# Performance work log

Hardware: AMD Instinct MI355X
Metric: run time of the kernel (lower is better)

Reference implementation:

```python
import jax, jax.numpy as jnp
import numpy as np

B, N, K, TC = 4, 4096, 16, 3
N_TAYLOR = 20  # 3rd-order Taylor monomials of (x,y,z): 1 + 3 + 6 + 10
CHANNELS = [(6, 32), (32, 64), (64, 128), (128, 256)]


def _taylor(rel):
    # rel: B,3,N,K relative coords -> B,20,N,K monomial basis up to degree 3
    x, y, z = rel[:, 0], rel[:, 1], rel[:, 2]
    one = jnp.ones_like(x)
    return jnp.stack([one, x, y, z,
                      x * x, x * y, x * z, y * y, y * z, z * z,
                      x * x * x, x * x * y, x * x * z, x * y * y, x * y * z,
                      x * z * z, y * y * y, y * y * z, y * z * z, z * z * z], axis=1)


def _group(feat, idx):
    # feat: B,C,N ; idx: B,N,K (int) -> B,C,N,K gathered neighbor features
    return jax.vmap(lambda f, i: f[:, i])(feat, idx)


def setup_inputs() -> dict:
    key = jax.random.key(0)
    ks = jax.random.split(key, 8)
    inp = {"pc": jax.random.normal(ks[0], (B, N, 6), dtype=jnp.float32)}
    for l, (cin, cout) in enumerate(CHANNELS, start=1):
        k1, k2 = jax.random.split(ks[l], 2)
        inp[f"w1_{l}"] = jax.random.normal(k1, (TC, N_TAYLOR), dtype=jnp.float32) * 0.1
        inp[f"b1_{l}"] = jnp.zeros((TC,), dtype=jnp.float32)
        fan_in = cin * TC * K
        inp[f"w2_{l}"] = jax.random.normal(k2, (cout, cin * TC, K), dtype=jnp.float32) * (1.0 / np.sqrt(fan_in))
        inp[f"b2_{l}"] = jnp.zeros((cout,), dtype=jnp.float32)
    return inp


def _forward(pc, params):
    pcT = pc.transpose(0, 2, 1)                 # B,6,N
    xyz = pcT[:, :3]                            # B,3,N
    # KNN graph: pairwise squared distances, top-k nearest (includes self)
    sq = jnp.sum(xyz * xyz, axis=1)             # B,N
    d2 = sq[:, :, None] + sq[:, None, :] - 2.0 * jnp.einsum('bcn,bcm->bnm', xyz, xyz)
    _, idx = jax.lax.top_k(-d2, K)              # B,N,K
    gxyz = _group(xyz, idx)                     # B,3,N,K
    rel = gxyz - xyz[:, :, :, None]             # B,3,N,K relative neighbor coords
    tay_basis = _taylor(rel)                    # B,20,N,K

    feat = pcT
    feats = []
    for (w1, b1, w2, b2) in params:
        # Taylor kernel weights: 1x1 conv over the 20 monomials -> TC channels
        tay = jnp.einsum('btnk,ct->bcnk', tay_basis, w1) + b1[None, :, None, None]  # B,TC,N,K
        gf = _group(feat, idx)                  # B,C,N,K
        C = gf.shape[1]
        fused = (gf[:, :, None] * tay[:, None]).reshape(B, C * TC, N, K)  # outer product
        # Conv2d(C*TC, out, kernel=(1,K)): contract channel and neighbor axes
        out = jnp.einsum('bcnk,ock->bon', fused, w2) + b2[None, :, None]
        feat = jax.nn.relu(out)                 # B,Cout,N
        feats.append(feat)

    point_feat = jnp.concatenate(feats, axis=1)  # B,480,N
    top2, _ = jax.lax.top_k(point_feat, 2)       # top-2 over N (last axis) -> B,480,2
    cat_feat = top2.reshape(B, -1)               # B,960
    return cat_feat, point_feat


def reference(pc, w1_1, b1_1, w2_1, b2_1, w1_2, b1_2, w2_2, b2_2,
              w1_3, b1_3, w2_3, b2_3, w1_4, b1_4, w2_4, b2_4):
    params = [(w1_1, b1_1, w2_1, b2_1), (w1_2, b1_2, w2_2, b2_2),
              (w1_3, b1_3, w2_3, b2_3), (w1_4, b1_4, w2_4, b2_4)]
    return _forward(pc, params)
```

## Files before the change

kernel.cpp:

```cpp
#include <hip/hip_runtime.h>
#include <hip/hip_fp16.h>
#include <cfloat>

#define BB 4
#define NN 4096
#define KK 16
#define NPTS (BB * NN)
#define NT48 (48 * NPTS)

typedef __attribute__((ext_vector_type(8))) _Float16 f16x8;
typedef __attribute__((ext_vector_type(4))) float f32x4;
typedef unsigned int u32;
typedef unsigned long long u64;

__device__ __forceinline__ short f2h(float v) {
  __half h = __float2half_rn(v);
  return __half_as_short(h);
}
__device__ __forceinline__ u32 mulh2(u32 a, __half2 t) {
  __half2 x = __hmul2(*(__half2*)&a, t);
  return *(u32*)&x;
}

__global__ __launch_bounds__(256) void pc2ft_kernel(const float* __restrict__ pc,
                                                    short* __restrict__ ft0,
                                                    float4* __restrict__ xyzq) {
  const int i = blockIdx.x * 256 + threadIdx.x;
  if (i >= NPTS) return;
  const float* s = pc + (size_t)i * 6;
  short* d = ft0 + (size_t)i * 8;
#pragma unroll
  for (int c = 0; c < 6; ++c) d[c] = f2h(s[c]);
  d[6] = 0; d[7] = 0;
  const float x = s[0], y = s[1], z = s[2];
  xyzq[i] = make_float4(x, y, z, fmaf(z, z, fmaf(y, y, x * x)));
}

__global__ __launch_bounds__(256) void knn_select(const float4* __restrict__ xyzq,
                                                  int* __restrict__ idx_out) {
  __shared__ float wT[4];
  __shared__ u64 list[128];
  __shared__ int lcnt;
  const int g = blockIdx.x;
  const int b = g >> 12;
  const int t = threadIdx.x;
  const int lane = t & 63;
  const float4* base = xyzq + (b << 12);
  const float4 q = xyzq[g];
  float d2v[16];
  float mymin = FLT_MAX;
#pragma unroll
  for (int i = 0; i < 16; ++i) {
    const float4 c = base[i * 256 + t];
    const float dot = fmaf(q.z, c.z, fmaf(q.y, c.y, q.x * c.x));
    d2v[i] = fmaf(-2.0f, dot, q.w + c.w);
    mymin = fminf(mymin, d2v[i]);
  }
  if (t == 0) lcnt = 0;
  float v = mymin;
#pragma unroll
  for (int k = 2; k <= 64; k <<= 1) {
#pragma unroll
    for (int j = k >> 1; j >= 1; j >>= 1) {
      const float o = __shfl_xor(v, j, 64);
      const bool take_min = (((lane & k) == 0) == ((lane & j) == 0));
      v = take_min ? fminf(v, o) : fmaxf(v, o);
    }
  }
  const float tw = __shfl(v, 15, 64);
  if (lane == 0) wT[t >> 6] = tw;
  __syncthreads();
  const float T = fminf(fminf(wT[0], wT[1]), fminf(wT[2], wT[3]));
#pragma unroll
  for (int i = 0; i < 16; ++i) {
    if (d2v[i] <= T) {
      const u32 bits = __float_as_uint(d2v[i]);
      const u32 key = bits ^ ((u32)((int)bits >> 31) | 0x80000000u);
      const int pos = atomicAdd(&lcnt, 1);
      if (pos < 128) list[pos] = ((u64)key << 32) | (u32)(i * 256 + t);
    }
  }
  __syncthreads();
  if (t < 128) {
    const int m = min(lcnt, 128);
    const u64 my = (t < m) ? list[t] : ~0ull;
    int rank = 0;
#pragma unroll 4
    for (int i = 0; i < m; ++i) rank += (list[i] < my) ? 1 : 0;
    if (t < m && rank < 16)
      idx_out[(size_t)g * KK + rank] = (int)(my & 0xFFFFFFFFull);
  }
}

__global__ __launch_bounds__(256) void wcvt_kernel(const float* __restrict__ w2,
                                                   short* __restrict__ wb,
                                                   int CIN, int COUT, int CPAD, int LOGC,
                                                   int total8) {
  const int i = blockIdx.x * 256 + threadIdx.x;
  if (i >= total8) return;
  const int q8 = i * 8;
  const int QT = CPAD * 48;
  const int o = q8 / QT;
  const int r = q8 - o * QT;
  const int kq = r >> LOGC;
  const int c0 = r & (CPAD - 1);
  const int tt = kq >> 4;
  const int k = kq & 15;
  short h[8];
#pragma unroll
  for (int j = 0; j < 8; ++j) {
    const int c = c0 + j;
    const float v = (o < COUT && c < CIN) ? w2[(size_t)o * CIN * 48 + (c * 3 + tt) * 16 + k] : 0.0f;
    h[j] = f2h(v);
  }
  short* d = wb + (size_t)o * QT + r;
#pragma unroll
  for (int j = 0; j < 8; ++j) d[j] = h[j];
}

__global__ __launch_bounds__(256) void taylor_kernel(
    const float* __restrict__ pc, const int* __restrict__ idx,
    const float* __restrict__ w1_1, const float* __restrict__ b1_1,
    const float* __restrict__ w1_2, const float* __restrict__ b1_2,
    const float* __restrict__ w1_3, const float* __restrict__ b1_3,
    const float* __restrict__ w1_4, const float* __restrict__ b1_4,
    float* __restrict__ tayg) {
  const int i = blockIdx.x * 256 + threadIdx.x;
  if (i >= NPTS * KK) return;
  const int p = i & (NPTS - 1);
  const int k = i >> 14;
  const int n = p & (NN - 1);
  const int b = p >> 12;
  const float* pcb = pc + (size_t)b * NN * 6;
  const int m = idx[(size_t)p * KK + k];
  const float x = pcb[m * 6 + 0] - pcb[n * 6 + 0];
  const float y = pcb[m * 6 + 1] - pcb[n * 6 + 1];
  const float z = pcb[m * 6 + 2] - pcb[n * 6 + 2];
  float tb[20];
  tb[0] = 1.0f; tb[1] = x; tb[2] = y; tb[3] = z;
  tb[4] = x * x; tb[5] = x * y; tb[6] = x * z;
  tb[7] = y * y; tb[8] = y * z; tb[9] = z * z;
  tb[10] = tb[4] * x; tb[11] = tb[4] * y; tb[12] = tb[4] * z;
  tb[13] = tb[5] * y; tb[14] = tb[5] * z; tb[15] = tb[6] * z;
  tb[16] = tb[7] * y; tb[17] = tb[7] * z; tb[18] = tb[8] * z; tb[19] = tb[9] * z;
  const float* w1s[4] = {w1_1, w1_2, w1_3, w1_4};
  const float* b1s[4] = {b1_1, b1_2, b1_3, b1_4};
#pragma unroll
  for (int l = 0; l < 4; ++l) {
    const float* w1 = w1s[l];
    const float* b1 = b1s[l];
#pragma unroll
    for (int c = 0; c < 3; ++c) {
      float s = b1[c];
#pragma unroll
      for (int j = 0; j < 20; ++j) s = fmaf(w1[c * 20 + j], tb[j], s);
      tayg[(size_t)(l * 48 + c * 16 + k) * NPTS + p] = s;
    }
  }
}

template <int CPAD, int LOGC, int COUT, int OTILE>
__global__ __launch_bounds__(256) void conv_mfma_kernel(
    const char* __restrict__ ftin,
    const short* __restrict__ wb,
    const float* __restrict__ b2,
    const float* __restrict__ tayg,
    const int* __restrict__ idx,
    float* __restrict__ pfout, int pfbstride,
    short* __restrict__ ftout, int CPADN) {
  constexpr int QTOT = CPAD * 48;
  constexpr int OUTER = QTOT / 64;
  constexpr int NJ = OTILE / 64;
  constexpr int PW = 16 * NJ;
  constexpr int NH = OTILE / 32;
  __shared__ __align__(16) short As[2][OTILE * 64];
  __shared__ __align__(16) short Bs[2][64 * 64];
  __shared__ __align__(16) unsigned short tayH[48 * 64];
  __shared__ int idxS[16 * 64];
  const int t = threadIdx.x;
  const int pbase = blockIdx.x * 64;
  const int obase = blockIdx.y * OTILE;
  const int b = pbase >> 12;
  const int nbase = pbase & (NN - 1);
  const int p_loc = t >> 2;
  const int sub = t & 3;
#pragma unroll
  for (int i = 0; i < 3; ++i) {
    const int f = i * 1024 + t * 4;
    const float4 tv4 = *(const float4*)&tayg[(size_t)(f >> 6) * NPTS + pbase + (f & 63)];
    ushort4 h4;
    h4.x = (unsigned short)f2h(tv4.x);
    h4.y = (unsigned short)f2h(tv4.y);
    h4.z = (unsigned short)f2h(tv4.z);
    h4.w = (unsigned short)f2h(tv4.w);
    *(ushort4*)&tayH[f] = h4;
  }
  {
    const int4 mi = *(const int4*)&idx[(size_t)(pbase + p_loc) * KK + sub * 4];
    const int gb = b << 12;
    idxS[(sub * 4 + 0) * 64 + p_loc] = (gb + mi.x) << (LOGC + 1);
    idxS[(sub * 4 + 1) * 64 + p_loc] = (gb + mi.y) << (LOGC + 1);
    idxS[(sub * 4 + 2) * 64 + p_loc] = (gb + mi.z) << (LOGC + 1);
    idxS[(sub * 4 + 3) * 64 + p_loc] = (gb + mi.w) << (LOGC + 1);
  }
  const int arow = t >> 3;
  const int apos = t & 7;
  const int aswz = (t >> 4) & 7;
  const short* awl[NH];
#pragma unroll
  for (int h = 0; h < NH; ++h)
    awl[h] = wb + (size_t)(obase + h * 32 + arow) * QTOT + ((apos ^ aswz) * 8);
  auto dmaA = [&](int o, int ph) {
#pragma unroll
    for (int h = 0; h < NH; ++h)
      __builtin_amdgcn_global_load_lds(
          (const __attribute__((address_space(1))) u32*)(awl[h] + o * 64),
          (__attribute__((address_space(3))) u32*)&As[ph][h * 2048 + t * 8], 16, 0, 0);
  };
  const int lane = t & 63;
  const int w = t >> 6;
  const int wm = (NJ == 2) ? (w & 1) : 0;
  const int wn = (NJ == 2) ? (w >> 1) : w;
  const int fr = lane & 15;
  const int fk = lane >> 4;
  const int rsw = (fr >> 1) & 7;
  const int bswz = (p_loc >> 1) & 7;
  f32x4 acc[4][NJ];
#pragma unroll
  for (int i = 0; i < 4; ++i)
#pragma unroll
    for (int j = 0; j < NJ; ++j) acc[i][j] = (f32x4)(0.0f);

  uint4 fv[2];
  unsigned short tvh[2];
  auto prefB = [&](int o) {
#pragma unroll
    for (int z = 0; z < 2; ++z) {
      const int q0 = o * 64 + z * 32 + sub * 8;
      const int kq = q0 >> LOGC;
      const int c0 = q0 & (CPAD - 1);
      const int moff = idxS[(kq & 15) * 64 + p_loc];
      tvh[z] = tayH[kq * 64 + p_loc];
      fv[z] = *(const uint4*)(ftin + moff + (c0 << 1));
    }
  };
  auto buildB = [&](int ph) {
#pragma unroll
    for (int z = 0; z < 2; ++z) {
      const __half2 t2 = __half2half2(__ushort_as_half(tvh[z]));
      const uint4 f = fv[z];
      uint4 r;
      r.x = mulh2(f.x, t2); r.y = mulh2(f.y, t2);
      r.z = mulh2(f.z, t2); r.w = mulh2(f.w, t2);
      const int pos = (z * 4 + sub) ^ bswz;
      *(uint4*)&Bs[ph][p_loc * 64 + pos * 8] = r;
    }
  };
  dmaA(0, 0);
  __syncthreads();
  prefB(0);
  buildB(0);
  __syncthreads();
#pragma unroll 1
  for (int o = 0; o < OUTER; ++o) {
    const int ph = o & 1;
    if (o + 1 < OUTER) { dmaA(o + 1, ph ^ 1); prefB(o + 1); }
#pragma unroll
    for (int z = 0; z < 2; ++z) {
      f16x8 af[4], bf[NJ];
      const int pos8 = ((z * 4 + fk) ^ rsw) * 8;
#pragma unroll
      for (int i = 0; i < 4; ++i)
        af[i] = *(const f16x8*)&As[ph][(wm * 64 + i * 16 + fr) * 64 + pos8];
#pragma unroll
      for (int j = 0; j < NJ; ++j)
        bf[j] = *(const f16x8*)&Bs[ph][(wn * PW + j * 16 + fr) * 64 + pos8];
#pragma unroll
      for (int i = 0; i < 4; ++i)
#pragma unroll
        for (int j = 0; j < NJ; ++j)
          acc[i][j] = __builtin_amdgcn_mfma_f32_16x16x32_f16(af[i], bf[j], acc[i][j], 0, 0, 0);
      if (z == 0 && o + 1 < OUTER) buildB(ph ^ 1);
    }
    if (o + 1 < OUTER) __syncthreads();
  }
  float* outb = pfout + (size_t)b * pfbstride;
#pragma unroll
  for (int i = 0; i < 4; ++i) {
    const int o0 = obase + wm * 64 + i * 16 + fk * 4;
    if (o0 < COUT) {
      const float4 b4 = *(const float4*)&b2[o0];
#pragma unroll
      for (int j = 0; j < NJ; ++j) {
        const int p_l = wn * PW + j * 16 + fr;
        const float v0 = fmaxf(acc[i][j][0] + b4.x, 0.0f);
        const float v1 = fmaxf(acc[i][j][1] + b4.y, 0.0f);
        const float v2 = fmaxf(acc[i][j][2] + b4.z, 0.0f);
        const float v3 = fmaxf(acc[i][j][3] + b4.w, 0.0f);
        outb[(size_t)(o0 + 0) * NN + nbase + p_l] = v0;
        outb[(size_t)(o0 + 1) * NN + nbase + p_l] = v1;
        outb[(size_t)(o0 + 2) * NN + nbase + p_l] = v2;
        outb[(size_t)(o0 + 3) * NN + nbase + p_l] = v3;
        if (ftout) {
          const __half2 h01 = __floats2half2_rn(v0, v1);
          const __half2 h23 = __floats2half2_rn(v2, v3);
          uint2 pk;
          pk.x = *(const u32*)&h01;
          pk.y = *(const u32*)&h23;
          *(uint2*)&ftout[(size_t)(pbase + p_l) * CPADN + o0] = pk;
        }
      }
    }
  }
}

__global__ __launch_bounds__(256) void top2_kernel(const float* __restrict__ pf,
                                                   float* __restrict__ cat) {
  const int row = blockIdx.x;
  const float* p = pf + (size_t)row * NN;
  float m1 = -FLT_MAX, m2 = -FLT_MAX;
  for (int i = threadIdx.x; i < NN; i += 256) {
    const float v = p[i];
    if (v > m1) { m2 = m1; m1 = v; }
    else if (v > m2) m2 = v;
  }
#pragma unroll
  for (int off = 32; off > 0; off >>= 1) {
    const float o1 = __shfl_down(m1, off, 64);
    const float o2 = __shfl_down(m2, off, 64);
    const float nm1 = fmaxf(m1, o1);
    const float nm2 = fmaxf(fminf(m1, o1), fmaxf(m2, o2));
    m1 = nm1; m2 = nm2;
  }
  __shared__ float s1[4], s2[4];
  const int wid = threadIdx.x >> 6;
  if ((threadIdx.x & 63) == 0) { s1[wid] = m1; s2[wid] = m2; }
  __syncthreads();
  if (threadIdx.x == 0) {
    m1 = s1[0]; m2 = s2[0];
#pragma unroll
    for (int w = 1; w < 4; ++w) {
      const float o1 = s1[w], o2 = s2[w];
      const float nm1 = fmaxf(m1, o1);
      const float nm2 = fmaxf(fminf(m1, o1), fmaxf(m2, o2));
      m1 = nm1; m2 = nm2;
    }
    const int b = row / 480, ch = row % 480;
    cat[b * 960 + ch * 2 + 0] = m1;
    cat[b * 960 + ch * 2 + 1] = m2;
  }
}

extern "C" void kernel_launch(void* const* d_in, const int* in_sizes, int n_in,
                              void* d_out, int out_size, void* d_ws, size_t ws_size,
                              hipStream_t stream) {
  const float* pc = (const float*)d_in[0];
  const float* w1s[4]; const float* b1s[4]; const float* w2s[4]; const float* b2s[4];
  for (int l = 0; l < 4; ++l) {
    w1s[l] = (const float*)d_in[1 + 4 * l];
    b1s[l] = (const float*)d_in[2 + 4 * l];
    w2s[l] = (const float*)d_in[3 + 4 * l];
    b2s[l] = (const float*)d_in[4 + 4 * l];
  }
  char* W = (char*)d_ws;
  int* idx = (int*)W;
  float* tayg = (float*)(W + 1048576);
  short* wb1 = (short*)(W + 13631488);
  short* wb2 = wb1 + 64 * 384;
  short* wb3 = wb2 + 64 * 1536;
  short* wb4 = wb3 + 128 * 3072;
  short* ft0 = (short*)(W + 17809408);
  short* ft1 = (short*)(W + 18071552);
  float4* xyzq = (float4*)(W + 1048576);
  short* ft2 = (short*)(W + 1048576);
  short* ft3 = (short*)(W + 1048576 + 2097152);
  float* cat = (float*)d_out;
  float* pf = (float*)d_out + BB * 960;
  const int pfstride = 480 * NN;

  pc2ft_kernel<<<dim3(NPTS / 256), 256, 0, stream>>>(pc, ft0, xyzq);
  knn_select<<<dim3(NPTS), 256, 0, stream>>>(xyzq, idx);
  wcvt_kernel<<<dim3((64 * 384 / 8 + 255) / 256), 256, 0, stream>>>(w2s[0], wb1, 6, 32, 8, 3, 64 * 384 / 8);
  wcvt_kernel<<<dim3((64 * 1536 / 8 + 255) / 256), 256, 0, stream>>>(w2s[1], wb2, 32, 64, 32, 5, 64 * 1536 / 8);
  wcvt_kernel<<<dim3((128 * 3072 / 8 + 255) / 256), 256, 0, stream>>>(w2s[2], wb3, 64, 128, 64, 6, 128 * 3072 / 8);
  wcvt_kernel<<<dim3((256 * 6144 / 8 + 255) / 256), 256, 0, stream>>>(w2s[3], wb4, 128, 256, 128, 7, 256 * 6144 / 8);
  taylor_kernel<<<dim3(NPTS * KK / 256), 256, 0, stream>>>(
      pc, idx, w1s[0], b1s[0], w1s[1], b1s[1], w1s[2], b1s[2], w1s[3], b1s[3], tayg);
  conv_mfma_kernel<8, 3, 32, 64><<<dim3(NPTS / 64, 1), 256, 0, stream>>>(
      (const char*)ft0, wb1, b2s[0], tayg + 0 * (size_t)NT48, idx,
      pf + (size_t)0 * NN, pfstride, ft1, 32);
  conv_mfma_kernel<32, 5, 64, 64><<<dim3(NPTS / 64, 1), 256, 0, stream>>>(
      (const char*)ft1, wb2, b2s[1], tayg + 1 * (size_t)NT48, idx,
      pf + (size_t)32 * NN, pfstride, ft2, 64);
  conv_mfma_kernel<64, 6, 128, 64><<<dim3(NPTS / 64, 2), 256, 0, stream>>>(
      (const char*)ft2, wb3, b2s[2], tayg + 2 * (size_t)NT48, idx,
      pf + (size_t)96 * NN, pfstride, ft3, 128);
  conv_mfma_kernel<128, 7, 256, 128><<<dim3(NPTS / 64, 2), 256, 0, stream>>>(
      (const char*)ft3, wb4, b2s[3], tayg + 3 * (size_t)NT48, idx,
      pf + (size_t)224 * NN, pfstride, nullptr, 0);
  top2_kernel<<<dim3(BB * 480), 256, 0, stream>>>(pf, cat);
}
```

Before: 367.6 us.

## Build conv B operand directly in registers and store Taylor weights as fp16

```diff
diff --git a/kernel.cpp b/kernel.cpp
--- a/kernel.cpp
+++ b/kernel.cpp
@@ -124,7 +124,7 @@
     const float* __restrict__ w1_2, const float* __restrict__ b1_2,
     const float* __restrict__ w1_3, const float* __restrict__ b1_3,
     const float* __restrict__ w1_4, const float* __restrict__ b1_4,
-    float* __restrict__ tayg) {
+    short* __restrict__ tayh) {
   const int i = blockIdx.x * 256 + threadIdx.x;
   if (i >= NPTS * KK) return;
   const int p = i & (NPTS - 1);
@@ -154,7 +154,7 @@
       float s = b1[c];
 #pragma unroll
       for (int j = 0; j < 20; ++j) s = fmaf(w1[c * 20 + j], tb[j], s);
-      tayg[(size_t)(l * 48 + c * 16 + k) * NPTS + p] = s;
+      tayh[(size_t)(l * 48 + c * 16 + k) * NPTS + p] = f2h(s);
     }
   }
 }
@@ -164,7 +164,7 @@
     const char* __restrict__ ftin,
     const short* __restrict__ wb,
     const float* __restrict__ b2,
-    const float* __restrict__ tayg,
+    const short* __restrict__ tayl,
     const int* __restrict__ idx,
     float* __restrict__ pfout, int pfbstride,
     short* __restrict__ ftout, int CPADN) {
@@ -174,7 +174,6 @@
   constexpr int PW = 16 * NJ;
   constexpr int NH = OTILE / 32;
   __shared__ __align__(16) short As[2][OTILE * 64];
-  __shared__ __align__(16) short Bs[2][64 * 64];
   __shared__ __align__(16) unsigned short tayH[48 * 64];
   __shared__ int idxS[16 * 64];
   const int t = threadIdx.x;
@@ -187,13 +186,8 @@
 #pragma unroll
   for (int i = 0; i < 3; ++i) {
     const int f = i * 1024 + t * 4;
-    const float4 tv4 = *(const float4*)&tayg[(size_t)(f >> 6) * NPTS + pbase + (f & 63)];
-    ushort4 h4;
-    h4.x = (unsigned short)f2h(tv4.x);
-    h4.y = (unsigned short)f2h(tv4.y);
-    h4.z = (unsigned short)f2h(tv4.z);
-    h4.w = (unsigned short)f2h(tv4.w);
-    *(ushort4*)&tayH[f] = h4;
+    *(ushort4*)&tayH[f] =
+        *(const ushort4*)&tayl[(size_t)(f >> 6) * NPTS + pbase + (f & 63)];
   }
   {
     const int4 mi = *(const int4*)&idx[(size_t)(pbase + p_loc) * KK + sub * 4];
@@ -224,63 +218,54 @@
   const int fr = lane & 15;
   const int fk = lane >> 4;
   const int rsw = (fr >> 1) & 7;
-  const int bswz = (p_loc >> 1) & 7;
   f32x4 acc[4][NJ];
 #pragma unroll
   for (int i = 0; i < 4; ++i)
 #pragma unroll
     for (int j = 0; j < NJ; ++j) acc[i][j] = (f32x4)(0.0f);
 
-  uint4 fv[2];
-  unsigned short tvh[2];
-  auto prefB = [&](int o) {
-#pragma unroll
-    for (int z = 0; z < 2; ++z) {
-      const int q0 = o * 64 + z * 32 + sub * 8;
-      const int kq = q0 >> LOGC;
-      const int c0 = q0 & (CPAD - 1);
-      const int moff = idxS[(kq & 15) * 64 + p_loc];
-      tvh[z] = tayH[kq * 64 + p_loc];
-      fv[z] = *(const uint4*)(ftin + moff + (c0 << 1));
-    }
-  };
-  auto buildB = [&](int ph) {
-#pragma unroll
-    for (int z = 0; z < 2; ++z) {
-      const __half2 t2 = __half2half2(__ushort_as_half(tvh[z]));
-      const uint4 f = fv[z];
-      uint4 r;
-      r.x = mulh2(f.x, t2); r.y = mulh2(f.y, t2);
-      r.z = mulh2(f.z, t2); r.w = mulh2(f.w, t2);
-      const int pos = (z * 4 + sub) ^ bswz;
-      *(uint4*)&Bs[ph][p_loc * 64 + pos * 8] = r;
-    }
+  uint4 bfv[2][2][NJ];
+  unsigned short tvh[2][2][NJ];
+  auto prefB = [&](int o, int slot) {
+#pragma unroll
+    for (int z = 0; z < 2; ++z)
+#pragma unroll
+      for (int j = 0; j < NJ; ++j) {
+        const int q0 = o * 64 + z * 32 + fk * 8;
+        const int kq = q0 >> LOGC;
+        const int c0 = q0 & (CPAD - 1);
+        const int p_l = wn * PW + j * 16 + fr;
+        const int moff = idxS[(kq & 15) * 64 + p_l];
+        tvh[slot][z][j] = tayH[kq * 64 + p_l];
+        bfv[slot][z][j] = *(const uint4*)(ftin + moff + (c0 << 1));
+      }
   };
   dmaA(0, 0);
   __syncthreads();
-  prefB(0);
-  buildB(0);
-  __syncthreads();
+  prefB(0, 0);
 #pragma unroll 1
   for (int o = 0; o < OUTER; ++o) {
     const int ph = o & 1;
-    if (o + 1 < OUTER) { dmaA(o + 1, ph ^ 1); prefB(o + 1); }
+    if (o + 1 < OUTER) { dmaA(o + 1, ph ^ 1); prefB(o + 1, ph ^ 1); }
 #pragma unroll
     for (int z = 0; z < 2; ++z) {
-      f16x8 af[4], bf[NJ];
+      f16x8 af[4];
       const int pos8 = ((z * 4 + fk) ^ rsw) * 8;
 #pragma unroll
       for (int i = 0; i < 4; ++i)
         af[i] = *(const f16x8*)&As[ph][(wm * 64 + i * 16 + fr) * 64 + pos8];
 #pragma unroll
-      for (int j = 0; j < NJ; ++j)
-        bf[j] = *(const f16x8*)&Bs[ph][(wn * PW + j * 16 + fr) * 64 + pos8];
-#pragma unroll
-      for (int i = 0; i < 4; ++i)
-#pragma unroll
-        for (int j = 0; j < NJ; ++j)
-          acc[i][j] = __builtin_amdgcn_mfma_f32_16x16x32_f16(af[i], bf[j], acc[i][j], 0, 0, 0);
-      if (z == 0 && o + 1 < OUTER) buildB(ph ^ 1);
+      for (int j = 0; j < NJ; ++j) {
+        const __half2 t2 = __half2half2(__ushort_as_half(tvh[ph][z][j]));
+        const uint4 fq = bfv[ph][z][j];
+        uint4 r;
+        r.x = mulh2(fq.x, t2); r.y = mulh2(fq.y, t2);
+        r.z = mulh2(fq.z, t2); r.w = mulh2(fq.w, t2);
+        const f16x8 bf = *(const f16x8*)&r;
+#pragma unroll
+        for (int i = 0; i < 4; ++i)
+          acc[i][j] = __builtin_amdgcn_mfma_f32_16x16x32_f16(af[i], bf, acc[i][j], 0, 0, 0);
+      }
     }
     if (o + 1 < OUTER) __syncthreads();
   }
@@ -364,7 +349,7 @@
   }
   char* W = (char*)d_ws;
   int* idx = (int*)W;
-  float* tayg = (float*)(W + 1048576);
+  short* tayh = (short*)(W + 1048576);
   short* wb1 = (short*)(W + 13631488);
   short* wb2 = wb1 + 64 * 384;
   short* wb3 = wb2 + 64 * 1536;
@@ -372,8 +357,8 @@
   short* ft0 = (short*)(W + 17809408);
   short* ft1 = (short*)(W + 18071552);
   float4* xyzq = (float4*)(W + 1048576);
-  short* ft2 = (short*)(W + 1048576);
-  short* ft3 = (short*)(W + 1048576 + 2097152);
+  short* ft2 = (short*)(W + 1048576 + 6291456);
+  short* ft3 = (short*)(W + 1048576 + 6291456 + 1048576);
   float* cat = (float*)d_out;
   float* pf = (float*)d_out + BB * 960;
   const int pfstride = 480 * NN;
@@ -385,18 +370,18 @@
   wcvt_kernel<<<dim3((128 * 3072 / 8 + 255) / 256), 256, 0, stream>>>(w2s[2], wb3, 64, 128, 64, 6, 128 * 3072 / 8);
   wcvt_kernel<<<dim3((256 * 6144 / 8 + 255) / 256), 256, 0, stream>>>(w2s[3], wb4, 128, 256, 128, 7, 256 * 6144 / 8);
   taylor_kernel<<<dim3(NPTS * KK / 256), 256, 0, stream>>>(
-      pc, idx, w1s[0], b1s[0], w1s[1], b1s[1], w1s[2], b1s[2], w1s[3], b1s[3], tayg);
+      pc, idx, w1s[0], b1s[0], w1s[1], b1s[1], w1s[2], b1s[2], w1s[3], b1s[3], tayh);
   conv_mfma_kernel<8, 3, 32, 64><<<dim3(NPTS / 64, 1), 256, 0, stream>>>(
-      (const char*)ft0, wb1, b2s[0], tayg + 0 * (size_t)NT48, idx,
+      (const char*)ft0, wb1, b2s[0], tayh + 0 * (size_t)NT48, idx,
       pf + (size_t)0 * NN, pfstride, ft1, 32);
   conv_mfma_kernel<32, 5, 64, 64><<<dim3(NPTS / 64, 1), 256, 0, stream>>>(
-      (const char*)ft1, wb2, b2s[1], tayg + 1 * (size_t)NT48, idx,
+      (const char*)ft1, wb2, b2s[1], tayh + 1 * (size_t)NT48, idx,
       pf + (size_t)32 * NN, pfstride, ft2, 64);
   conv_mfma_kernel<64, 6, 128, 64><<<dim3(NPTS / 64, 2), 256, 0, stream>>>(
-      (const char*)ft2, wb3, b2s[2], tayg + 2 * (size_t)NT48, idx,
+      (const char*)ft2, wb3, b2s[2], tayh + 2 * (size_t)NT48, idx,
       pf + (size_t)96 * NN, pfstride, ft3, 128);
   conv_mfma_kernel<128, 7, 256, 128><<<dim3(NPTS / 64, 2), 256, 0, stream>>>(
-      (const char*)ft3, wb4, b2s[3], tayg + 3 * (size_t)NT48, idx,
+      (const char*)ft3, wb4, b2s[3], tayh + 3 * (size_t)NT48, idx,
       pf + (size_t)224 * NN, pfstride, nullptr, 0);
   top2_kernel<<<dim3(BB * 480), 256, 0, stream>>>(pf, cat);
 }
```

Result: slower. 602.5 us (+63.9%).

## Store Taylor weights in fp16 and split-K warps in the 128-wide conv tile

Applied to the files above, without the earlier changes.

```diff
diff --git a/kernel.cpp b/kernel.cpp
--- a/kernel.cpp
+++ b/kernel.cpp
@@ -124,7 +124,7 @@
     const float* __restrict__ w1_2, const float* __restrict__ b1_2,
     const float* __restrict__ w1_3, const float* __restrict__ b1_3,
     const float* __restrict__ w1_4, const float* __restrict__ b1_4,
-    float* __restrict__ tayg) {
+    short* __restrict__ tayh) {
   const int i = blockIdx.x * 256 + threadIdx.x;
   if (i >= NPTS * KK) return;
   const int p = i & (NPTS - 1);
@@ -154,7 +154,7 @@
       float s = b1[c];
 #pragma unroll
       for (int j = 0; j < 20; ++j) s = fmaf(w1[c * 20 + j], tb[j], s);
-      tayg[(size_t)(l * 48 + c * 16 + k) * NPTS + p] = s;
+      tayh[(size_t)(l * 48 + c * 16 + k) * NPTS + p] = f2h(s);
     }
   }
 }
@@ -164,14 +164,14 @@
     const char* __restrict__ ftin,
     const short* __restrict__ wb,
     const float* __restrict__ b2,
-    const float* __restrict__ tayg,
+    const short* __restrict__ tayl,
     const int* __restrict__ idx,
     float* __restrict__ pfout, int pfbstride,
     short* __restrict__ ftout, int CPADN) {
   constexpr int QTOT = CPAD * 48;
   constexpr int OUTER = QTOT / 64;
   constexpr int NJ = OTILE / 64;
-  constexpr int PW = 16 * NJ;
+  constexpr int NJC = (NJ == 2) ? 4 : 1;
   constexpr int NH = OTILE / 32;
   __shared__ __align__(16) short As[2][OTILE * 64];
   __shared__ __align__(16) short Bs[2][64 * 64];
@@ -187,13 +187,8 @@
 #pragma unroll
   for (int i = 0; i < 3; ++i) {
     const int f = i * 1024 + t * 4;
-    const float4 tv4 = *(const float4*)&tayg[(size_t)(f >> 6) * NPTS + pbase + (f & 63)];
-    ushort4 h4;
-    h4.x = (unsigned short)f2h(tv4.x);
-    h4.y = (unsigned short)f2h(tv4.y);
-    h4.z = (unsigned short)f2h(tv4.z);
-    h4.w = (unsigned short)f2h(tv4.w);
-    *(ushort4*)&tayH[f] = h4;
+    *(ushort4*)&tayH[f] =
+        *(const ushort4*)&tayl[(size_t)(f >> 6) * NPTS + pbase + (f & 63)];
   }
   {
     const int4 mi = *(const int4*)&idx[(size_t)(pbase + p_loc) * KK + sub * 4];
@@ -220,16 +215,17 @@
   const int lane = t & 63;
   const int w = t >> 6;
   const int wm = (NJ == 2) ? (w & 1) : 0;
-  const int wn = (NJ == 2) ? (w >> 1) : w;
+  const int ksw = (NJ == 2) ? (w >> 1) : 0;
+  const int wn = (NJ == 2) ? 0 : w;
   const int fr = lane & 15;
   const int fk = lane >> 4;
   const int rsw = (fr >> 1) & 7;
   const int bswz = (p_loc >> 1) & 7;
-  f32x4 acc[4][NJ];
+  f32x4 acc[4][NJC];
 #pragma unroll
   for (int i = 0; i < 4; ++i)
 #pragma unroll
-    for (int j = 0; j < NJ; ++j) acc[i][j] = (f32x4)(0.0f);
+    for (int j = 0; j < NJC; ++j) acc[i][j] = (f32x4)(0.0f);
 
   uint4 fv[2];
   unsigned short tvh[2];
@@ -265,24 +261,59 @@
   for (int o = 0; o < OUTER; ++o) {
     const int ph = o & 1;
     if (o + 1 < OUTER) { dmaA(o + 1, ph ^ 1); prefB(o + 1); }
-#pragma unroll
-    for (int z = 0; z < 2; ++z) {
-      f16x8 af[4], bf[NJ];
-      const int pos8 = ((z * 4 + fk) ^ rsw) * 8;
+    if constexpr (NJ == 2) {
+      f16x8 af[4], bf[4];
+      const int pos8 = ((ksw * 4 + fk) ^ rsw) * 8;
 #pragma unroll
       for (int i = 0; i < 4; ++i)
         af[i] = *(const f16x8*)&As[ph][(wm * 64 + i * 16 + fr) * 64 + pos8];
 #pragma unroll
-      for (int j = 0; j < NJ; ++j)
-        bf[j] = *(const f16x8*)&Bs[ph][(wn * PW + j * 16 + fr) * 64 + pos8];
+      for (int j = 0; j < 4; ++j)
+        bf[j] = *(const f16x8*)&Bs[ph][(j * 16 + fr) * 64 + pos8];
+      if (o + 1 < OUTER) buildB(ph ^ 1);
 #pragma unroll
       for (int i = 0; i < 4; ++i)
 #pragma unroll
-        for (int j = 0; j < NJ; ++j)
+        for (int j = 0; j < 4; ++j)
           acc[i][j] = __builtin_amdgcn_mfma_f32_16x16x32_f16(af[i], bf[j], acc[i][j], 0, 0, 0);
-      if (z == 0 && o + 1 < OUTER) buildB(ph ^ 1);
+    } else {
+#pragma unroll
+      for (int z = 0; z < 2; ++z) {
+        f16x8 af[4], bf;
+        const int pos8 = ((z * 4 + fk) ^ rsw) * 8;
+#pragma unroll
+        for (int i = 0; i < 4; ++i)
+          af[i] = *(const f16x8*)&As[ph][(i * 16 + fr) * 64 + pos8];
+        bf = *(const f16x8*)&Bs[ph][(wn * 16 + fr) * 64 + pos8];
+        if (z == 0 && o + 1 < OUTER) buildB(ph ^ 1);
+#pragma unroll
+        for (int i = 0; i < 4; ++i)
+          acc[i][0] = __builtin_amdgcn_mfma_f32_16x16x32_f16(af[i], bf, acc[i][0], 0, 0, 0);
+      }
     }
     if (o + 1 < OUTER) __syncthreads();
+  }
+  if constexpr (NJ == 2) {
+    __syncthreads();
+    float* red = (float*)(&As[0][0]) + wm * 4096;
+    if (ksw == 1) {
+#pragma unroll
+      for (int i = 0; i < 4; ++i)
+#pragma unroll
+        for (int j = 0; j < 4; ++j)
+#pragma unroll
+          for (int r = 0; r < 4; ++r)
+            red[((i * 4 + j) * 4 + r) * 64 + lane] = acc[i][j][r];
+    }
+    __syncthreads();
+    if (ksw == 1) return;
+#pragma unroll
+    for (int i = 0; i < 4; ++i)
+#pragma unroll
+      for (int j = 0; j < 4; ++j)
+#pragma unroll
+        for (int r = 0; r < 4; ++r)
+          acc[i][j][r] += red[((i * 4 + j) * 4 + r) * 64 + lane];
   }
   float* outb = pfout + (size_t)b * pfbstride;
 #pragma unroll
@@ -291,8 +322,8 @@
     if (o0 < COUT) {
       const float4 b4 = *(const float4*)&b2[o0];
 #pragma unroll
-      for (int j = 0; j < NJ; ++j) {
-        const int p_l = wn * PW + j * 16 + fr;
+      for (int j = 0; j < NJC; ++j) {
+        const int p_l = (NJ == 2) ? (j * 16 + fr) : (wn * 16 + fr);
         const float v0 = fmaxf(acc[i][j][0] + b4.x, 0.0f);
         const float v1 = fmaxf(acc[i][j][1] + b4.y, 0.0f);
         const float v2 = fmaxf(acc[i][j][2] + b4.z, 0.0f);
@@ -364,7 +395,7 @@
   }
   char* W = (char*)d_ws;
   int* idx = (int*)W;
-  float* tayg = (float*)(W + 1048576);
+  short* tayh = (short*)(W + 1048576);
   short* wb1 = (short*)(W + 13631488);
   short* wb2 = wb1 + 64 * 384;
   short* wb3 = wb2 + 64 * 1536;
@@ -372,8 +403,8 @@
   short* ft0 = (short*)(W + 17809408);
   short* ft1 = (short*)(W + 18071552);
   float4* xyzq = (float4*)(W + 1048576);
-  short* ft2 = (short*)(W + 1048576);
-  short* ft3 = (short*)(W + 1048576 + 2097152);
+  short* ft2 = (short*)(W + 1048576 + 6291456);
+  short* ft3 = (short*)(W + 1048576 + 6291456 + 1048576);
   float* cat = (float*)d_out;
   float* pf = (float*)d_out + BB * 960;
   const int pfstride = 480 * NN;
@@ -385,18 +416,18 @@
   wcvt_kernel<<<dim3((128 * 3072 / 8 + 255) / 256), 256, 0, stream>>>(w2s[2], wb3, 64, 128, 64, 6, 128 * 3072 / 8);
   wcvt_kernel<<<dim3((256 * 6144 / 8 + 255) / 256), 256, 0, stream>>>(w2s[3], wb4, 128, 256, 128, 7, 256 * 6144 / 8);
   taylor_kernel<<<dim3(NPTS * KK / 256), 256, 0, stream>>>(
-      pc, idx, w1s[0], b1s[0], w1s[1], b1s[1], w1s[2], b1s[2], w1s[3], b1s[3], tayg);
+      pc, idx, w1s[0], b1s[0], w1s[1], b1s[1], w1s[2], b1s[2], w1s[3], b1s[3], tayh);
   conv_mfma_kernel<8, 3, 32, 64><<<dim3(NPTS / 64, 1), 256, 0, stream>>>(
-      (const char*)ft0, wb1, b2s[0], tayg + 0 * (size_t)NT48, idx,
+      (const char*)ft0, wb1, b2s[0], tayh + 0 * (size_t)NT48, idx,
       pf + (size_t)0 * NN, pfstride, ft1, 32);
   conv_mfma_kernel<32, 5, 64, 64><<<dim3(NPTS / 64, 1), 256, 0, stream>>>(
-      (const char*)ft1, wb2, b2s[1], tayg + 1 * (size_t)NT48, idx,
+      (const char*)ft1, wb2, b2s[1], tayh + 1 * (size_t)NT48, idx,
       pf + (size_t)32 * NN, pfstride, ft2, 64);
   conv_mfma_kernel<64, 6, 128, 64><<<dim3(NPTS / 64, 2), 256, 0, stream>>>(
-      (const char*)ft2, wb3, b2s[2], tayg + 2 * (size_t)NT48, idx,
+      (const char*)ft2, wb3, b2s[2], tayh + 2 * (size_t)NT48, idx,
       pf + (size_t)96 * NN, pfstride, ft3, 128);
   conv_mfma_kernel<128, 7, 256, 128><<<dim3(NPTS / 64, 2), 256, 0, stream>>>(
-      (const char*)ft3, wb4, b2s[3], tayg + 3 * (size_t)NT48, idx,
+      (const char*)ft3, wb4, b2s[3], tayh + 3 * (size_t)NT48, idx,
       pf + (size_t)224 * NN, pfstride, nullptr, 0);
   top2_kernel<<<dim3(BB * 480), 256, 0, stream>>>(pf, cat);
 }
```

New measurement: 357.0 us. 1.03x faster.
